# Performance work log

Hardware: AMD Instinct MI355X
Metric: run time of the kernel (lower is better)

Reference implementation:

```python
import jax, jax.numpy as jnp
import numpy as np

# index_map: 16 contiguous groups of 8 old classes each (group_id = old_idx // 8)
C_OLD, C_NEW = 128, 16
GROUP_IDS = jnp.arange(C_OLD) // (C_OLD // C_NEW)          # [C_old]
GROUP_MAT = jax.nn.one_hot(GROUP_IDS, C_NEW, dtype=jnp.float32)  # [C_old, C_new]
EPS = 1e-8


def setup_inputs() -> dict:
    key = jax.random.key(0)
    k1, k2 = jax.random.split(key)
    B, N = 8, 65536
    inputs = jax.random.normal(k1, (B, N, C_OLD), dtype=jnp.float32)   # stacked inputs_list
    # targets are percentage distributions (module divides by 100)
    targets = jax.random.uniform(k2, (B, C_NEW), dtype=jnp.float32) * 100.0
    return {"inputs": inputs, "targets": targets}


def reference(inputs, targets):
    # per-item: softmax over old classes, grouped sum into new classes
    probs = jax.nn.softmax(inputs, axis=-1)                 # [B, N, C_old]
    grouped = jnp.einsum('bnc,cg->bng', probs, GROUP_MAT)   # [B, N, C_new] grouped sum
    avg = jnp.mean(grouped, axis=1)                         # [B, C_new]
    smoothed_p = jax.nn.softmax(avg, axis=-1)               # [B, C_new]
    smoothed_t = jax.nn.softmax(targets / 100.0, axis=-1)   # [B, C_new]
    log_p = jnp.log(smoothed_p + EPS)
    # KLDivLoss(reduction='batchmean') on a 1-D input divides by its first dim (C_new)
    kl = jnp.sum(smoothed_t * (jnp.log(smoothed_t) - log_p), axis=-1) / C_NEW  # [B]
    return jnp.mean(kl)
```

## Files before the change

kernel.cpp:

```cpp
#include <hip/hip_runtime.h>

#define C_OLD 128
#define C_NEW 16
#define N_ROWS 65536
#define BATCH 8
#define BLOCKS_PER_B 256
#define ROWS_PER_BLOCK (N_ROWS / BLOCKS_PER_B)
#define THREADS 256
#define HALFWAVES (THREADS / 32)
#define ITERS (ROWS_PER_BLOCK / HALFWAVES)
#define L2E 1.44269504088896340736f

__global__ __launch_bounds__(THREADS) void grouped_partial(
    const float* __restrict__ in, float* __restrict__ part) {
  const int bid = blockIdx.x;
  const int b   = bid / BLOCKS_PER_B;
  const int rb  = bid % BLOCKS_PER_B;
  const int tid = threadIdx.x;
  const int h   = tid >> 5;
  const int m   = tid & 31;

  const long long row0 = (long long)b * N_ROWS + (long long)rb * ROWS_PER_BLOCK + h;
  const float4* __restrict__ p = (const float4*)(in + row0 * C_OLD) + m;
  const int strideF4 = HALFWAVES * (C_OLD / 4);

  float acc = 0.f;
  #pragma unroll 4
  for (int it = 0; it < ITERS; ++it) {
    float4 v = p[(long long)it * strideF4];

    float e = __builtin_amdgcn_exp2f(v.x * L2E) +
              __builtin_amdgcn_exp2f(v.y * L2E) +
              __builtin_amdgcn_exp2f(v.z * L2E) +
              __builtin_amdgcn_exp2f(v.w * L2E);

    float g2 = e + __shfl_xor(e, 1, 32);
    float t = g2;
    #pragma unroll
    for (int off = 2; off < 32; off <<= 1)
      t += __shfl_xor(t, off, 32);

    acc += g2 * __builtin_amdgcn_rcpf(t);
  }

  __shared__ float sacc[HALFWAVES][C_NEW];
  if ((m & 1) == 0) sacc[h][m >> 1] = acc;
  __syncthreads();

  if (tid < C_NEW) {
    float s = 0.f;
    #pragma unroll
    for (int k = 0; k < HALFWAVES; ++k) s += sacc[k][tid];
    part[bid * C_NEW + tid] = s;
  }
}

__global__ __launch_bounds__(1024) void final_kl(
    const float* __restrict__ part, const float* __restrict__ targets,
    float* __restrict__ out) {
  const int tid = threadIdx.x;
  const int b   = tid >> 7;
  const int sub = (tid >> 4) & 7;
  const int g   = tid & 15;

  float s = 0.f;
  for (int k = sub; k < BLOCKS_PER_B; k += 8)
    s += part[(b * BLOCKS_PER_B + k) * C_NEW + g];

  __shared__ float red[BATCH][8][C_NEW];
  red[b][sub][g] = s;
  __syncthreads();

  if (tid < BATCH * C_NEW) {
    const int bb = tid >> 4;
    const int gg = tid & 15;
    float sum = 0.f;
    #pragma unroll
    for (int k = 0; k < 8; ++k) sum += red[bb][k][gg];
    const float avg = sum / (float)N_ROWS;

    float mx = avg;
    #pragma unroll
    for (int off = 1; off < 16; off <<= 1) mx = fmaxf(mx, __shfl_xor(mx, off, 16));
    float e = expf(avg - mx);
    float den = e;
    #pragma unroll
    for (int off = 1; off < 16; off <<= 1) den += __shfl_xor(den, off, 16);
    const float pr = e / den;

    const float tg = targets[bb * C_NEW + gg] * 0.01f;
    float tmx = tg;
    #pragma unroll
    for (int off = 1; off < 16; off <<= 1) tmx = fmaxf(tmx, __shfl_xor(tmx, off, 16));
    float te = expf(tg - tmx);
    float tden = te;
    #pragma unroll
    for (int off = 1; off < 16; off <<= 1) tden += __shfl_xor(tden, off, 16);
    const float tp = te / tden;

    float term = tp * (logf(tp) - logf(pr + 1e-8f));
    #pragma unroll
    for (int off = 1; off < 16; off <<= 1) term += __shfl_xor(term, off, 16);

    __shared__ float kb[BATCH];
    if (gg == 0) kb[bb] = term / (float)C_NEW;
    __syncthreads();
    if (tid == 0) {
      float tot = 0.f;
      #pragma unroll
      for (int k = 0; k < BATCH; ++k) tot += kb[k];
      out[0] = tot / (float)BATCH;
    }
  }
}

extern "C" void kernel_launch(void* const* d_in, const int* in_sizes, int n_in,
                              void* d_out, int out_size, void* d_ws, size_t ws_size,
                              hipStream_t stream) {
  const float* inputs  = (const float*)d_in[0];
  const float* targets = (const float*)d_in[1];
  float* out  = (float*)d_out;
  float* part = (float*)d_ws;

  const int nblocks = BATCH * BLOCKS_PER_B;
  grouped_partial<<<nblocks, THREADS, 0, stream>>>(inputs, part);
  final_kl<<<1, 1024, 0, stream>>>(part, targets, out);
}
```

Before: 54.41 us.

## Fuse final KL reduction into main kernel via last-block atomic counter

Merges the two-kernel pipeline into one kernel: each block publishes its partial sums, increments a global counter, and the last block to finish performs the cross-block reduction and KL computation. This removes the second kernel launch and its dependency gap, but adds a memset launch for the counter. The final reduction now runs on 256 threads instead of 1024. The memory ordering relies on an agent-scope relaxed atomic store plus atomicAdd, which may be weaker than a proper release/acquire fence.

Result: slower. 62.82 us (+15.4%).

```diff
diff --git a/kernel.cpp b/kernel.cpp
--- a/kernel.cpp
+++ b/kernel.cpp
@@ -5,29 +5,30 @@
 #define N_ROWS 65536
 #define BATCH 8
 #define BLOCKS_PER_B 256
+#define NBLOCKS (BATCH * BLOCKS_PER_B)
 #define ROWS_PER_BLOCK (N_ROWS / BLOCKS_PER_B)
 #define THREADS 256
 #define HALFWAVES (THREADS / 32)
 #define ITERS (ROWS_PER_BLOCK / HALFWAVES)
 #define L2E 1.44269504088896340736f
 
-__global__ __launch_bounds__(THREADS) void grouped_partial(
-    const float* __restrict__ in, float* __restrict__ part) {
+__global__ __launch_bounds__(THREADS) void grouped_fused(
+    const float* __restrict__ in, const float* __restrict__ targets,
+    float* __restrict__ out, float* __restrict__ part, int* __restrict__ counter) {
   const int bid = blockIdx.x;
-  const int b   = bid / BLOCKS_PER_B;
-  const int rb  = bid % BLOCKS_PER_B;
+  const int b   = bid >> 8;
+  const int rb  = bid & (BLOCKS_PER_B - 1);
   const int tid = threadIdx.x;
   const int h   = tid >> 5;
   const int m   = tid & 31;
 
   const long long row0 = (long long)b * N_ROWS + (long long)rb * ROWS_PER_BLOCK + h;
   const float4* __restrict__ p = (const float4*)(in + row0 * C_OLD) + m;
-  const int strideF4 = HALFWAVES * (C_OLD / 4);
 
   float acc = 0.f;
   #pragma unroll 4
   for (int it = 0; it < ITERS; ++it) {
-    float4 v = p[(long long)it * strideF4];
+    float4 v = p[it * (HALFWAVES * (C_OLD / 4))];
 
     float e = __builtin_amdgcn_exp2f(v.x * L2E) +
               __builtin_amdgcn_exp2f(v.y * L2E) +
@@ -51,32 +52,44 @@
     float s = 0.f;
     #pragma unroll
     for (int k = 0; k < HALFWAVES; ++k) s += sacc[k][tid];
-    part[bid * C_NEW + tid] = s;
+    __hip_atomic_store(&part[bid * C_NEW + tid], s, __ATOMIC_RELAXED,
+                       __HIP_MEMORY_SCOPE_AGENT);
   }
-}
-
-__global__ __launch_bounds__(1024) void final_kl(
-    const float* __restrict__ part, const float* __restrict__ targets,
-    float* __restrict__ out) {
-  const int tid = threadIdx.x;
-  const int b   = tid >> 7;
-  const int sub = (tid >> 4) & 7;
-  const int g   = tid & 15;
-
-  float s = 0.f;
-  for (int k = sub; k < BLOCKS_PER_B; k += 8)
-    s += part[(b * BLOCKS_PER_B + k) * C_NEW + g];
-
-  __shared__ float red[BATCH][8][C_NEW];
-  red[b][sub][g] = s;
   __syncthreads();
 
+  __shared__ int isLast;
+  if (tid == 0)
+    isLast = (atomicAdd(counter, 1) == NBLOCKS - 1);
+  __syncthreads();
+  if (!isLast) return;
+
+  float accB[BATCH];
+  #pragma unroll
+  for (int i = 0; i < BATCH; ++i) accB[i] = 0.f;
+  #pragma unroll
+  for (int j = 0; j < 128; ++j)
+    accB[j >> 4] += part[j * 256 + tid];
+
+  #pragma unroll
+  for (int bb = 0; bb < BATCH; ++bb) {
+    accB[bb] += __shfl_xor(accB[bb], 16, 64);
+    accB[bb] += __shfl_xor(accB[bb], 32, 64);
+  }
+
+  __shared__ float red[4][BATCH][C_NEW];
+  {
+    const int w = tid >> 6, lane = tid & 63;
+    if (lane < C_NEW) {
+      #pragma unroll
+      for (int bb = 0; bb < BATCH; ++bb) red[w][bb][lane] = accB[bb];
+    }
+  }
+  __syncthreads();
+
+  __shared__ float kb[BATCH];
   if (tid < BATCH * C_NEW) {
-    const int bb = tid >> 4;
-    const int gg = tid & 15;
-    float sum = 0.f;
-    #pragma unroll
-    for (int k = 0; k < 8; ++k) sum += red[bb][k][gg];
+    const int bb = tid >> 4, g = tid & 15;
+    const float sum = red[0][bb][g] + red[1][bb][g] + red[2][bb][g] + red[3][bb][g];
     const float avg = sum / (float)N_ROWS;
 
     float mx = avg;
@@ -88,7 +101,7 @@
     for (int off = 1; off < 16; off <<= 1) den += __shfl_xor(den, off, 16);
     const float pr = e / den;
 
-    const float tg = targets[bb * C_NEW + gg] * 0.01f;
+    const float tg = targets[bb * C_NEW + g] * 0.01f;
     float tmx = tg;
     #pragma unroll
     for (int off = 1; off < 16; off <<= 1) tmx = fmaxf(tmx, __shfl_xor(tmx, off, 16));
@@ -102,15 +115,14 @@
     #pragma unroll
     for (int off = 1; off < 16; off <<= 1) term += __shfl_xor(term, off, 16);
 
-    __shared__ float kb[BATCH];
-    if (gg == 0) kb[bb] = term / (float)C_NEW;
-    __syncthreads();
-    if (tid == 0) {
-      float tot = 0.f;
-      #pragma unroll
-      for (int k = 0; k < BATCH; ++k) tot += kb[k];
-      out[0] = tot / (float)BATCH;
-    }
+    if (g == 0) kb[bb] = term / (float)C_NEW;
+  }
+  __syncthreads();
+  if (tid == 0) {
+    float tot = 0.f;
+    #pragma unroll
+    for (int k = 0; k < BATCH; ++k) tot += kb[k];
+    out[0] = tot / (float)BATCH;
   }
 }
 
@@ -120,9 +132,9 @@
   const float* inputs  = (const float*)d_in[0];
   const float* targets = (const float*)d_in[1];
   float* out  = (float*)d_out;
-  float* part = (float*)d_ws;
+  int*   counter = (int*)d_ws;
+  float* part = (float*)((char*)d_ws + 1024);
 
-  const int nblocks = BATCH * BLOCKS_PER_B;
-  grouped_partial<<<nblocks, THREADS, 0, stream>>>(inputs, part);
-  final_kl<<<1, 1024, 0, stream>>>(part, targets, out);
+  hipMemsetAsync(counter, 0, sizeof(int), stream);
+  grouped_fused<<<NBLOCKS, THREADS, 0, stream>>>(inputs, targets, out, part, counter);
 }
```
